# Kernel tuning notes

Hardware: AMD Instinct MI355X
Metric: run time of the kernel (lower is better)

The kernel has to match this reference:

```python
import jax, jax.numpy as jnp
import numpy as np


def setup_inputs() -> dict:
    key = jax.random.key(0)
    k1, k2 = jax.random.split(key)
    L, O, N, D = 512, 512, 64, 512
    x = jax.random.normal(k1, (L, N, D), dtype=jnp.float32)
    upfold = jax.random.normal(k2, (O, N, D), dtype=jnp.float32)
    return {"x": x, "upfold": upfold}


def reference(x, upfold):
    # x: [L, N, D], upfold: [O, N, D]
    D = x.shape[-1]
    scale = 1.0 / jnp.sqrt(jnp.asarray(D, dtype=x.dtype))
    # affinities: [L, O, N]
    affinities = jnp.einsum('lnd,ond->lon', x, upfold) * scale
    # sigmoid-attention (no softmax normalization), centered at 0
    weights = jax.nn.sigmoid(affinities) - 0.5
    # features: [L, N, D]
    features = jnp.einsum('lon,ond->lnd', weights, upfold)
    return features
```

## Files before the change

kernel.cpp:

```cpp
#include <hip/hip_runtime.h>
#include <hip/hip_bf16.h>
#include <stdint.h>


typedef __attribute__((ext_vector_type(8))) short short8;
typedef __attribute__((ext_vector_type(4))) float f32x4;

__device__ __forceinline__ uint16_t f2bf(float f) {
    uint32_t u = __builtin_bit_cast(uint32_t, f);
    uint32_t r = u + 0x7FFFu + ((u >> 16) & 1u);
    return (uint16_t)(r >> 16);
}
__device__ __forceinline__ uint32_t cvt2(float a, float b) {
    return (uint32_t)f2bf(a) | ((uint32_t)f2bf(b) << 16);
}

__global__ __launch_bounds__(256) void kPrepUp(const float* __restrict__ up,
                                               uint16_t* __restrict__ ub,
                                               uint16_t* __restrict__ ut) {
    __shared__ float tile[64][65];
    int b = blockIdx.x;
    int n = b >> 6, r = b & 63;
    int o0 = (r >> 3) << 6, d0 = (r & 7) << 6;
    int tid = threadIdx.x;
    int i  = tid >> 2;
    int jq = (tid & 3) << 4;

    const float* src = up + ((size_t)(o0 + i) * 64 + n) * 512 + d0 + jq;
    float v[16];
    #pragma unroll
    for (int c = 0; c < 16; c += 4) {
        float4 q = *reinterpret_cast<const float4*>(src + c);
        v[c] = q.x; v[c+1] = q.y; v[c+2] = q.z; v[c+3] = q.w;
        tile[i][jq+c] = q.x; tile[i][jq+c+1] = q.y;
        tile[i][jq+c+2] = q.z; tile[i][jq+c+3] = q.w;
    }
    uint32_t pk[8];
    if (ub) {
        #pragma unroll
        for (int c = 0; c < 8; ++c) pk[c] = cvt2(v[2*c], v[2*c+1]);
        uint16_t* udst = ub + ((size_t)n * 512 + o0 + i) * 512 + d0 + jq;
        *reinterpret_cast<uint4*>(udst)     = *reinterpret_cast<const uint4*>(pk);
        *reinterpret_cast<uint4*>(udst + 8) = *reinterpret_cast<const uint4*>(pk + 4);
    }
    __syncthreads();
    #pragma unroll
    for (int c = 0; c < 8; ++c) pk[c] = cvt2(tile[jq + 2*c][i], tile[jq + 2*c + 1][i]);
    uint16_t* tdst = ut + ((size_t)n * 512 + d0 + i) * 512 + o0 + jq;
    *reinterpret_cast<uint4*>(tdst)     = *reinterpret_cast<const uint4*>(pk);
    *reinterpret_cast<uint4*>(tdst + 8) = *reinterpret_cast<const uint4*>(pk + 4);
}

__global__ __launch_bounds__(256) void kPrepX(const float* __restrict__ x,
                                              uint16_t* __restrict__ xb) {
    int b = blockIdx.x;
    int tid = threadIdx.x;
    int row = b * 4 + (tid >> 6);
    int l = row >> 6, n = row & 63;
    int d0 = (tid & 63) * 8;
    const float* src = x + (size_t)row * 512 + d0;
    float4 v0 = *reinterpret_cast<const float4*>(src);
    float4 v1 = *reinterpret_cast<const float4*>(src + 4);
    uint32_t pk[4] = {cvt2(v0.x, v0.y), cvt2(v0.z, v0.w),
                      cvt2(v1.x, v1.y), cvt2(v1.z, v1.w)};
    *reinterpret_cast<uint4*>(xb + ((size_t)n * 512 + l) * 512 + d0) =
        *reinterpret_cast<const uint4*>(pk);
}

template<int MODE>
__global__ __launch_bounds__(256) void kGemmT(const uint16_t* __restrict__ A,
                                              const uint16_t* __restrict__ B,
                                              void* __restrict__ outp) {
    __shared__ uint16_t As[2][8192];
    __shared__ uint16_t Bs[2][8192];
    int d = blockIdx.x;
    int n  = (d & 7) * 8 + (d >> 7);
    int t  = (d >> 3) & 15;
    int l0 = (t >> 2) << 7, c0 = (t & 3) << 7;
    int tid = threadIdx.x, lane = tid & 63, wid = tid >> 6;
    int wr = wid >> 1, wc = wid & 1;

    const char* An = (const char*)(A + (size_t)n * 262144);
    const char* Bn = (const char*)(B + (size_t)n * 262144);
    int rsub  = lane >> 3;
    int sbyte = ((lane & 7) ^ rsub) << 4;
    const char* gA = An + (size_t)(l0 + wid * 32 + rsub) * 1024 + sbyte;
    const char* gB = Bn + (size_t)(c0 + wid * 32 + rsub) * 1024 + sbyte;

    f32x4 acc[4][4];
    #pragma unroll
    for (int m = 0; m < 4; ++m)
        #pragma unroll
        for (int nf = 0; nf < 4; ++nf) acc[m][nf] = (f32x4)(0.f);

    auto STAGE = [&](int buf, int kt) {
        const char* pA = gA + kt * 128;
        const char* pB = gB + kt * 128;
        uint16_t* lA = &As[buf][wid * 2048];
        uint16_t* lB = &Bs[buf][wid * 2048];
        #pragma unroll
        for (int j = 0; j < 4; ++j) {
            __builtin_amdgcn_global_load_lds(
                (const __attribute__((address_space(1))) uint32_t*)(pA + j * 8192),
                (__attribute__((address_space(3))) uint32_t*)(lA + j * 512), 16, 0, 0);
            __builtin_amdgcn_global_load_lds(
                (const __attribute__((address_space(1))) uint32_t*)(pB + j * 8192),
                (__attribute__((address_space(3))) uint32_t*)(lB + j * 512), 16, 0, 0);
        }
    };

    STAGE(0, 0);
    asm volatile("s_waitcnt vmcnt(0)" ::: "memory");
    __builtin_amdgcn_s_barrier();

    int cur = 0;
    for (int kt = 0; kt < 8; ++kt) {
        if (kt < 7) STAGE(cur ^ 1, kt + 1);
        #pragma unroll
        for (int kk = 0; kk < 2; ++kk) {
            short8 a[4], bb[4];
            int kbyte = kk * 64 + ((lane >> 4) * 16);
            #pragma unroll
            for (int m = 0; m < 4; ++m) {
                int row = wr * 64 + m * 16 + (lane & 15);
                int off = row * 128 + (kbyte ^ ((row & 7) << 4));
                a[m] = *reinterpret_cast<const short8*>((const char*)As[cur] + off);
            }
            #pragma unroll
            for (int nf = 0; nf < 4; ++nf) {
                int row = wc * 64 + nf * 16 + (lane & 15);
                int off = row * 128 + (kbyte ^ ((row & 7) << 4));
                bb[nf] = *reinterpret_cast<const short8*>((const char*)Bs[cur] + off);
            }
            #pragma unroll
            for (int m = 0; m < 4; ++m)
                #pragma unroll
                for (int nf = 0; nf < 4; ++nf)
                    acc[m][nf] = __builtin_amdgcn_mfma_f32_16x16x32_bf16(
                        a[m], bb[nf], acc[m][nf], 0, 0, 0);
        }
        if (kt < 7) {
            asm volatile("s_waitcnt vmcnt(0)" ::: "memory");
            __builtin_amdgcn_s_barrier();
        }
        cur ^= 1;
    }

    if constexpr (MODE == 1) {
        uint16_t* Wn = (uint16_t*)outp + (size_t)n * 262144;
        const float scale = 0.044194173824159216f;
        #pragma unroll
        for (int m = 0; m < 4; ++m) {
            int lrow0 = l0 + wr * 64 + m * 16 + ((lane >> 4) << 2);
            #pragma unroll
            for (int nf = 0; nf < 4; ++nf) {
                int ocol = c0 + wc * 64 + nf * 16 + (lane & 15);
                #pragma unroll
                for (int r = 0; r < 4; ++r) {
                    float aff = acc[m][nf][r] * scale;
                    float w = 1.f / (1.f + __expf(-aff)) - 0.5f;
                    Wn[(size_t)(lrow0 + r) * 512 + ocol] = f2bf(w);
                }
            }
        }
    } else {
        float* On = (float*)outp;
        #pragma unroll
        for (int m = 0; m < 4; ++m) {
            int lrow0 = l0 + wr * 64 + m * 16 + ((lane >> 4) << 2);
            #pragma unroll
            for (int nf = 0; nf < 4; ++nf) {
                int dcol = c0 + wc * 64 + nf * 16 + (lane & 15);
                #pragma unroll
                for (int r = 0; r < 4; ++r)
                    On[((size_t)(lrow0 + r) * 64 + n) * 512 + dcol] = acc[m][nf][r];
            }
        }
    }
}

__global__ __launch_bounds__(256) void kGemm1f32(const float* __restrict__ x,
                                                 const float* __restrict__ up,
                                                 uint16_t* __restrict__ W) {
    __shared__ uint16_t As[128 * 64];
    __shared__ uint16_t Bs[128 * 64];
    int b   = blockIdx.x;
    int n   = b >> 4;
    int t   = b & 15;
    int l0  = (t >> 2) << 7, o0 = (t & 3) << 7;
    int tid = threadIdx.x, lane = tid & 63, wid = tid >> 6;
    int wr = wid >> 1, wc = wid & 1;

    f32x4 acc[4][4];
    #pragma unroll
    for (int m = 0; m < 4; ++m)
        #pragma unroll
        for (int nf = 0; nf < 4; ++nf) acc[m][nf] = (f32x4)(0.f);

    int srow = tid >> 1;
    int kh   = (tid & 1) * 32;
    int swz  = (srow & 7) << 4;
    const float* aSrc = x  + ((size_t)(l0 + srow) * 64 + n) * 512 + kh;
    const float* bSrc = up + ((size_t)(o0 + srow) * 64 + n) * 512 + kh;

    for (int kt = 0; kt < 8; ++kt) {
        __syncthreads();
        const float* pA = aSrc + kt * 64;
        const float* pB = bSrc + kt * 64;
        #pragma unroll
        for (int c2 = 0; c2 < 4; ++c2) {
            float4 a0 = *reinterpret_cast<const float4*>(pA + c2 * 8);
            float4 a1 = *reinterpret_cast<const float4*>(pA + c2 * 8 + 4);
            float4 b0 = *reinterpret_cast<const float4*>(pB + c2 * 8);
            float4 b1 = *reinterpret_cast<const float4*>(pB + c2 * 8 + 4);
            uint32_t pa[4] = {cvt2(a0.x,a0.y), cvt2(a0.z,a0.w), cvt2(a1.x,a1.y), cvt2(a1.z,a1.w)};
            uint32_t pb[4] = {cvt2(b0.x,b0.y), cvt2(b0.z,b0.w), cvt2(b1.x,b1.y), cvt2(b1.z,b1.w)};
            int off = srow * 128 + (((kh * 2) + c2 * 16) ^ swz);
            *reinterpret_cast<uint4*>((char*)As + off) = *reinterpret_cast<const uint4*>(pa);
            *reinterpret_cast<uint4*>((char*)Bs + off) = *reinterpret_cast<const uint4*>(pb);
        }
        __syncthreads();
        #pragma unroll
        for (int kk = 0; kk < 2; ++kk) {
            short8 a[4], bf[4];
            int kbyte = kk * 64 + ((lane >> 4) * 16);
            #pragma unroll
            for (int m = 0; m < 4; ++m) {
                int row = wr * 64 + m * 16 + (lane & 15);
                int off = row * 128 + (kbyte ^ ((row & 7) << 4));
                a[m] = *reinterpret_cast<const short8*>((char*)As + off);
            }
            #pragma unroll
            for (int nf = 0; nf < 4; ++nf) {
                int row = wc * 64 + nf * 16 + (lane & 15);
                int off = row * 128 + (kbyte ^ ((row & 7) << 4));
                bf[nf] = *reinterpret_cast<const short8*>((char*)Bs + off);
            }
            #pragma unroll
            for (int m = 0; m < 4; ++m)
                #pragma unroll
                for (int nf = 0; nf < 4; ++nf)
                    acc[m][nf] = __builtin_amdgcn_mfma_f32_16x16x32_bf16(
                        a[m], bf[nf], acc[m][nf], 0, 0, 0);
        }
    }
    const float scale = 0.044194173824159216f;
    #pragma unroll
    for (int m = 0; m < 4; ++m) {
        int lrow0 = l0 + wr * 64 + m * 16 + ((lane >> 4) << 2);
        #pragma unroll
        for (int nf = 0; nf < 4; ++nf) {
            int ocol = o0 + wc * 64 + nf * 16 + (lane & 15);
            #pragma unroll
            for (int r = 0; r < 4; ++r) {
                float aff = acc[m][nf][r] * scale;
                float w = 1.f / (1.f + __expf(-aff)) - 0.5f;
                W[((size_t)n * 512 + (lrow0 + r)) * 512 + ocol] = f2bf(w);
            }
        }
    }
}

__global__ __launch_bounds__(256) void kNaive(const float* __restrict__ x,
                                              const float* __restrict__ up,
                                              float* __restrict__ out) {
    __shared__ float xr[512];
    __shared__ float w[512];
    int b = blockIdx.x;
    int l = b >> 6, n = b & 63;
    int tid = threadIdx.x;
    const float* xrow = x + ((size_t)l * 64 + n) * 512;
    xr[tid] = xrow[tid];
    xr[tid + 256] = xrow[tid + 256];
    __syncthreads();
    const float scale = 0.044194173824159216f;
    #pragma unroll
    for (int oo = 0; oo < 2; ++oo) {
        int o = tid + oo * 256;
        const float* ur = up + ((size_t)o * 64 + n) * 512;
        float s = 0.f;
        for (int dd = 0; dd < 512; ++dd) s += xr[dd] * ur[dd];
        w[o] = 1.f / (1.f + __expf(-s * scale)) - 0.5f;
    }
    __syncthreads();
    #pragma unroll
    for (int dd = 0; dd < 2; ++dd) {
        int d = tid + dd * 256;
        float f = 0.f;
        for (int o = 0; o < 512; ++o)
            f += w[o] * up[((size_t)o * 64 + n) * 512 + d];
        out[((size_t)l * 64 + n) * 512 + d] = f;
    }
}

extern "C" void kernel_launch(void* const* d_in, const int* in_sizes, int n_in,
                              void* d_out, int out_size, void* d_ws, size_t ws_size,
                              hipStream_t stream) {
    const float* x  = (const float*)d_in[0];
    const float* up = (const float*)d_in[1];
    float* out = (float*)d_out;

    const size_t MB32 = (size_t)64 * 512 * 512 * 2;
    if (ws_size >= 4 * MB32) {
        uint16_t* XB = (uint16_t*)d_ws;
        uint16_t* UB = XB + 16777216;
        uint16_t* UT = UB + 16777216;
        uint16_t* W  = UT + 16777216;
        kPrepUp<<<4096, 256, 0, stream>>>(up, UB, UT);
        kPrepX <<<8192, 256, 0, stream>>>(x, XB);
        kGemmT<1><<<1024, 256, 0, stream>>>(XB, UB, W);
        kGemmT<2><<<1024, 256, 0, stream>>>(W, UT, out);
    } else if (ws_size >= 2 * MB32) {
        uint16_t* UT = (uint16_t*)d_ws;
        uint16_t* W  = UT + 16777216;
        kPrepUp<<<4096, 256, 0, stream>>>(up, nullptr, UT);
        kGemm1f32<<<1024, 256, 0, stream>>>(x, up, W);
        kGemmT<2><<<1024, 256, 0, stream>>>(W, UT, out);
    } else {
        kNaive<<<512 * 64, 256, 0, stream>>>(x, up, out);
    }
}
```

Before: 112.6 us.

## Use 256x256 tiles with 512-thread blocks for both bf16 GEMMs

Replaces the 128x128-tile, 4-wave GEMM kernel with a 256x256-tile, 8-wave version. Each wave now computes 128x64 outputs with 8x4 MFMA accumulators, and the main path launches 256 blocks, one per CU. The goal is more operand reuse per LDS/global load and fewer blocks. The cost is double-buffered LDS of about 128KB per block and 128 accumulator registers per thread, which leaves low occupancy and little latency hiding. A separate single-buffered 128x128 kernel is added for the fallback workspace path.

```diff
diff --git a/kernel.cpp b/kernel.cpp
--- a/kernel.cpp
+++ b/kernel.cpp
@@ -68,17 +68,17 @@
 }
 
 template<int MODE>
-__global__ __launch_bounds__(256) void kGemmT(const uint16_t* __restrict__ A,
-                                              const uint16_t* __restrict__ B,
-                                              void* __restrict__ outp) {
-    __shared__ uint16_t As[2][8192];
-    __shared__ uint16_t Bs[2][8192];
-    int d = blockIdx.x;
-    int n  = (d & 7) * 8 + (d >> 7);
-    int t  = (d >> 3) & 15;
-    int l0 = (t >> 2) << 7, c0 = (t & 3) << 7;
+__global__ __launch_bounds__(512) void kGemm256(const uint16_t* __restrict__ A,
+                                                const uint16_t* __restrict__ B,
+                                                void* __restrict__ outp) {
+    __shared__ uint16_t As[2][16384];
+    __shared__ uint16_t Bs[2][16384];
+    int bid = blockIdx.x;
+    int n  = (bid & 7) * 8 + (bid >> 5);
+    int t  = (bid >> 3) & 3;
+    int l0 = (t >> 1) << 8, c0 = (t & 1) << 8;
     int tid = threadIdx.x, lane = tid & 63, wid = tid >> 6;
-    int wr = wid >> 1, wc = wid & 1;
+    int wr = wid >> 2, wc = wid & 3;
 
     const char* An = (const char*)(A + (size_t)n * 262144);
     const char* Bn = (const char*)(B + (size_t)n * 262144);
@@ -87,9 +87,9 @@
     const char* gA = An + (size_t)(l0 + wid * 32 + rsub) * 1024 + sbyte;
     const char* gB = Bn + (size_t)(c0 + wid * 32 + rsub) * 1024 + sbyte;
 
-    f32x4 acc[4][4];
-    #pragma unroll
-    for (int m = 0; m < 4; ++m)
+    f32x4 acc[8][4];
+    #pragma unroll
+    for (int m = 0; m < 8; ++m)
         #pragma unroll
         for (int nf = 0; nf < 4; ++nf) acc[m][nf] = (f32x4)(0.f);
 
@@ -113,27 +113,29 @@
     asm volatile("s_waitcnt vmcnt(0)" ::: "memory");
     __builtin_amdgcn_s_barrier();
 
-    int cur = 0;
     for (int kt = 0; kt < 8; ++kt) {
+        const int cur = kt & 1;
         if (kt < 7) STAGE(cur ^ 1, kt + 1);
+        const uint16_t* Ac = As[cur];
+        const uint16_t* Bc = Bs[cur];
         #pragma unroll
         for (int kk = 0; kk < 2; ++kk) {
-            short8 a[4], bb[4];
+            short8 a[8], bb[4];
             int kbyte = kk * 64 + ((lane >> 4) * 16);
             #pragma unroll
-            for (int m = 0; m < 4; ++m) {
-                int row = wr * 64 + m * 16 + (lane & 15);
-                int off = row * 128 + (kbyte ^ ((row & 7) << 4));
-                a[m] = *reinterpret_cast<const short8*>((const char*)As[cur] + off);
-            }
-            #pragma unroll
             for (int nf = 0; nf < 4; ++nf) {
                 int row = wc * 64 + nf * 16 + (lane & 15);
                 int off = row * 128 + (kbyte ^ ((row & 7) << 4));
-                bb[nf] = *reinterpret_cast<const short8*>((const char*)Bs[cur] + off);
-            }
-            #pragma unroll
-            for (int m = 0; m < 4; ++m)
+                bb[nf] = *reinterpret_cast<const short8*>((const char*)Bc + off);
+            }
+            #pragma unroll
+            for (int m = 0; m < 8; ++m) {
+                int row = wr * 128 + m * 16 + (lane & 15);
+                int off = row * 128 + (kbyte ^ ((row & 7) << 4));
+                a[m] = *reinterpret_cast<const short8*>((const char*)Ac + off);
+            }
+            #pragma unroll
+            for (int m = 0; m < 8; ++m)
                 #pragma unroll
                 for (int nf = 0; nf < 4; ++nf)
                     acc[m][nf] = __builtin_amdgcn_mfma_f32_16x16x32_bf16(
@@ -143,15 +145,14 @@
             asm volatile("s_waitcnt vmcnt(0)" ::: "memory");
             __builtin_amdgcn_s_barrier();
         }
-        cur ^= 1;
     }
 
     if constexpr (MODE == 1) {
         uint16_t* Wn = (uint16_t*)outp + (size_t)n * 262144;
         const float scale = 0.044194173824159216f;
         #pragma unroll
-        for (int m = 0; m < 4; ++m) {
-            int lrow0 = l0 + wr * 64 + m * 16 + ((lane >> 4) << 2);
+        for (int m = 0; m < 8; ++m) {
+            int lrow0 = l0 + wr * 128 + m * 16 + ((lane >> 4) << 2);
             #pragma unroll
             for (int nf = 0; nf < 4; ++nf) {
                 int ocol = c0 + wc * 64 + nf * 16 + (lane & 15);
@@ -166,8 +167,8 @@
     } else {
         float* On = (float*)outp;
         #pragma unroll
-        for (int m = 0; m < 4; ++m) {
-            int lrow0 = l0 + wr * 64 + m * 16 + ((lane >> 4) << 2);
+        for (int m = 0; m < 8; ++m) {
+            int lrow0 = l0 + wr * 128 + m * 16 + ((lane >> 4) << 2);
             #pragma unroll
             for (int nf = 0; nf < 4; ++nf) {
                 int dcol = c0 + wc * 64 + nf * 16 + (lane & 15);
@@ -257,6 +258,82 @@
                 float w = 1.f / (1.f + __expf(-aff)) - 0.5f;
                 W[((size_t)n * 512 + (lrow0 + r)) * 512 + ocol] = f2bf(w);
             }
+        }
+    }
+}
+
+__global__ __launch_bounds__(256) void kGemm2Mid(const uint16_t* __restrict__ W,
+                                                 const uint16_t* __restrict__ ut,
+                                                 float* __restrict__ out) {
+    __shared__ uint16_t As[8192];
+    __shared__ uint16_t Bs[8192];
+    int d = blockIdx.x;
+    int n  = (d & 7) * 8 + (d >> 7);
+    int t  = (d >> 3) & 15;
+    int l0 = (t >> 2) << 7, c0 = (t & 3) << 7;
+    int tid = threadIdx.x, lane = tid & 63, wid = tid >> 6;
+    int wr = wid >> 1, wc = wid & 1;
+
+    const char* An = (const char*)(W  + (size_t)n * 262144);
+    const char* Bn = (const char*)(ut + (size_t)n * 262144);
+    int rsub  = lane >> 3;
+    int sbyte = ((lane & 7) ^ rsub) << 4;
+    const char* gA = An + (size_t)(l0 + wid * 32 + rsub) * 1024 + sbyte;
+    const char* gB = Bn + (size_t)(c0 + wid * 32 + rsub) * 1024 + sbyte;
+    uint16_t* lA = As + wid * 2048;
+    uint16_t* lB = Bs + wid * 2048;
+
+    f32x4 acc[4][4];
+    #pragma unroll
+    for (int m = 0; m < 4; ++m)
+        #pragma unroll
+        for (int nf = 0; nf < 4; ++nf) acc[m][nf] = (f32x4)(0.f);
+
+    for (int kt = 0; kt < 8; ++kt) {
+        if (kt) __syncthreads();
+        #pragma unroll
+        for (int j = 0; j < 4; ++j) {
+            __builtin_amdgcn_global_load_lds(
+                (const __attribute__((address_space(1))) uint32_t*)(gA + kt * 128 + j * 8192),
+                (__attribute__((address_space(3))) uint32_t*)(lA + j * 512), 16, 0, 0);
+            __builtin_amdgcn_global_load_lds(
+                (const __attribute__((address_space(1))) uint32_t*)(gB + kt * 128 + j * 8192),
+                (__attribute__((address_space(3))) uint32_t*)(lB + j * 512), 16, 0, 0);
+        }
+        __syncthreads();
+        #pragma unroll
+        for (int kk = 0; kk < 2; ++kk) {
+            short8 a[4], bb[4];
+            int kbyte = kk * 64 + ((lane >> 4) * 16);
+            #pragma unroll
+            for (int m = 0; m < 4; ++m) {
+                int row = wr * 64 + m * 16 + (lane & 15);
+                int off = row * 128 + (kbyte ^ ((row & 7) << 4));
+                a[m] = *reinterpret_cast<const short8*>((const char*)As + off);
+            }
+            #pragma unroll
+            for (int nf = 0; nf < 4; ++nf) {
+                int row = wc * 64 + nf * 16 + (lane & 15);
+                int off = row * 128 + (kbyte ^ ((row & 7) << 4));
+                bb[nf] = *reinterpret_cast<const short8*>((const char*)Bs + off);
+            }
+            #pragma unroll
+            for (int m = 0; m < 4; ++m)
+                #pragma unroll
+                for (int nf = 0; nf < 4; ++nf)
+                    acc[m][nf] = __builtin_amdgcn_mfma_f32_16x16x32_bf16(
+                        a[m], bb[nf], acc[m][nf], 0, 0, 0);
+        }
+    }
+    #pragma unroll
+    for (int m = 0; m < 4; ++m) {
+        int lrow0 = l0 + wr * 64 + m * 16 + ((lane >> 4) << 2);
+        #pragma unroll
+        for (int nf = 0; nf < 4; ++nf) {
+            int dcol = c0 + wc * 64 + nf * 16 + (lane & 15);
+            #pragma unroll
+            for (int r = 0; r < 4; ++r)
+                out[((size_t)(lrow0 + r) * 64 + n) * 512 + dcol] = acc[m][nf][r];
         }
     }
 }
@@ -308,14 +385,14 @@
         uint16_t* W  = UT + 16777216;
         kPrepUp<<<4096, 256, 0, stream>>>(up, UB, UT);
         kPrepX <<<8192, 256, 0, stream>>>(x, XB);
-        kGemmT<1><<<1024, 256, 0, stream>>>(XB, UB, W);
-        kGemmT<2><<<1024, 256, 0, stream>>>(W, UT, out);
+        kGemm256<1><<<256, 512, 0, stream>>>(XB, UB, W);
+        kGemm256<2><<<256, 512, 0, stream>>>(W, UT, out);
     } else if (ws_size >= 2 * MB32) {
         uint16_t* UT = (uint16_t*)d_ws;
         uint16_t* W  = UT + 16777216;
         kPrepUp<<<4096, 256, 0, stream>>>(up, nullptr, UT);
         kGemm1f32<<<1024, 256, 0, stream>>>(x, up, W);
-        kGemmT<2><<<1024, 256, 0, stream>>>(W, UT, out);
+        kGemm2Mid<<<1024, 256, 0, stream>>>(W, UT, out);
     } else {
         kNaive<<<512 * 64, 256, 0, stream>>>(x, up, out);
     }
```

Result: faster. 110.1 us (-2.2%).
